# Kernel tuning notes

Measured on AMD Instinct MI355X. Metric: run time of the kernel, lower is better.

## Reference

```python
import jax, jax.numpy as jnp
import numpy as np

N, M, D = 32768, 4096, 256   # tokens, codebook_size, dim_feature
COMMITMENT_WEIGHT = 0.25


def setup_inputs() -> dict:
    key = jax.random.key(0)
    kx, ke = jax.random.split(key)
    x = jax.random.normal(kx, (N, D), dtype=jnp.float32)
    # learnable codebook (kaiming-uniform in torch; normal is fine for a numeric baseline)
    embed = jax.random.normal(ke, (M, D), dtype=jnp.float32) * (D ** -0.5)
    return {"x": x, "embed": embed}


def reference(x, embed):
    # argmin over squared distances == argmin over sqrt distances (monotone),
    # matching l2_dist(...).argmin(dim=1) in the original KeOps path.
    x2 = jnp.sum(x * x, axis=-1, keepdims=True)          # [N,1]
    e2 = jnp.sum(embed * embed, axis=-1)                 # [M]
    d2 = x2 - 2.0 * (x @ embed.T) + e2[None, :]          # [N,M]
    idx = jnp.argmin(d2, axis=1)                         # [N] code assignment

    q = embed[idx]                                       # codebook gather [N,D]

    # straight-through estimator: forward value is q, gradient flows to x
    quantized = x + jax.lax.stop_gradient(q - x)

    # commitment loss beta*||sg(x_q) - x||^2 + codebook loss ||x_q - sg(x)||^2
    commit_loss = COMMITMENT_WEIGHT * jnp.mean((jax.lax.stop_gradient(q) - x) ** 2)
    codebook_loss = jnp.mean((q - jax.lax.stop_gradient(x)) ** 2)
    loss = commit_loss + codebook_loss

    # cluster sizes via scatter-add (bincount) and perplexity
    counts = jnp.zeros((M,), jnp.float32).at[idx].add(1.0)
    probs = counts / counts.sum()
    perplexity = jnp.exp(-jnp.sum(probs * jnp.log(probs + 1e-10)))

    return quantized, idx, loss, perplexity
```

## Files before the change

### kernel.cpp

```cpp
#include <hip/hip_runtime.h>
#include <hip/hip_bf16.h>
#include <math.h>

#define NTOK 32768
#define MCB  4096
#define DDIM 256
#define NGATHER 8192

typedef __attribute__((ext_vector_type(8))) short bf16x8;
typedef __attribute__((ext_vector_type(4))) float f32x4;

__device__ __forceinline__ unsigned short f2bf_rne(float f) {
  unsigned int u = __float_as_uint(f);
  unsigned int r = u + 0x7FFFu + ((u >> 16) & 1u);
  return (unsigned short)(r >> 16);
}

__device__ __forceinline__ float bf2f(unsigned short h) {
  return __uint_as_float(((unsigned int)h) << 16);
}

__device__ __forceinline__ void cvt8(const float* f, bf16x8& hi, bf16x8& lo) {
  #pragma unroll
  for (int j = 0; j < 8; ++j) {
    unsigned short hs = f2bf_rne(f[j]);
    float lf = f[j] - bf2f(hs);
    hi[j] = (short)hs;
    lo[j] = (short)f2bf_rne(lf);
  }
}

__device__ __forceinline__ void load_lds16(const void* g, void* l) {
  __builtin_amdgcn_global_load_lds(
      (const __attribute__((address_space(1))) void*)g,
      (__attribute__((address_space(3))) void*)l, 16, 0, 0);
}

__global__ __launch_bounds__(256) void vq_prep_kernel(
    const float* __restrict__ embed, char* __restrict__ ehi,
    char* __restrict__ elo, float* __restrict__ e2) {
  const int id = blockIdx.x * 256 + threadIdx.x;
  const int row = id >> 5;
  const int c = id & 31;
  const float* ep = embed + (size_t)row * DDIM + c * 8;
  const float4 f0 = *(const float4*)(ep);
  const float4 f1 = *(const float4*)(ep + 4);
  float f[8] = {f0.x, f0.y, f0.z, f0.w, f1.x, f1.y, f1.z, f1.w};
  bf16x8 h, l;
  cvt8(f, h, l);
  const size_t off = (size_t)row * 512 + (size_t)(((c ^ (row & 7)) * 16));
  *(bf16x8*)(ehi + off) = h;
  *(bf16x8*)(elo + off) = l;
  float s = 0.0f;
  #pragma unroll
  for (int j = 0; j < 8; ++j) s += f[j] * f[j];
  #pragma unroll
  for (int m = 1; m < 32; m <<= 1) s += __shfl_xor(s, m, 64);
  if (c == 0) e2[row] = s;
}

__global__ __launch_bounds__(256, 2) void vq_main_kernel(
    const float* __restrict__ x, const char* __restrict__ ehi,
    const char* __restrict__ elo, const float* __restrict__ e2,
    float* __restrict__ ws_score, int* __restrict__ ws_idx) {
  __shared__ char lds[65536];
  const int tid = threadIdx.x;
  const int lane = tid & 63;
  const int wv = tid >> 6;
  const int split = blockIdx.x;
  const int row0 = blockIdx.y * 128 + wv * 32;
  const int colbase = split * 1024;
  const int l15 = lane & 15;
  const int l4 = lane >> 4;

  bf16x8 axh[2][8], axl[2][8];
  #pragma unroll
  for (int rf = 0; rf < 2; ++rf) {
    const float* xp = x + (size_t)(row0 + rf * 16 + l15) * DDIM + l4 * 8;
    #pragma unroll
    for (int ks = 0; ks < 8; ++ks) {
      float4 f0 = *(const float4*)(xp + ks * 32);
      float4 f1 = *(const float4*)(xp + ks * 32 + 4);
      float f[8] = {f0.x, f0.y, f0.z, f0.w, f1.x, f1.y, f1.z, f1.w};
      cvt8(f, axh[rf][ks], axl[rf][ks]);
    }
  }

  float minv[2][4];
  int mini[2][4];
  #pragma unroll
  for (int rf = 0; rf < 2; ++rf)
    #pragma unroll
    for (int r = 0; r < 4; ++r) { minv[rf][r] = 3.0e38f; mini[rf][r] = 0; }

  for (int ct = 0; ct < 16; ++ct) {
    __syncthreads();
    {
      const size_t tb = (size_t)(colbase + ct * 64) * 512 + (size_t)tid * 16;
      const char* ghi = ehi + tb;
      const char* glo = elo + tb;
      #pragma unroll
      for (int i = 0; i < 8; ++i) {
        load_lds16(ghi + i * 4096, lds + tid * 16 + i * 4096);
        load_lds16(glo + i * 4096, lds + 32768 + tid * 16 + i * 4096);
      }
    }
    __syncthreads();

    f32x4 acc[2][4];
    #pragma unroll
    for (int rf = 0; rf < 2; ++rf)
      #pragma unroll
      for (int cf = 0; cf < 4; ++cf) {
        f32x4 z = {0.0f, 0.0f, 0.0f, 0.0f};
        acc[rf][cf] = z;
      }

    #pragma unroll
    for (int ks = 0; ks < 8; ++ks) {
      bf16x8 bh[4], bl[4];
      #pragma unroll
      for (int cf = 0; cf < 4; ++cf) {
        const int brow = cf * 16 + l15;
        const int off = brow * 512 + (((ks * 4 + l4) ^ (brow & 7)) * 16);
        bh[cf] = *(const bf16x8*)(lds + off);
        bl[cf] = *(const bf16x8*)(lds + 32768 + off);
      }
      #pragma unroll
      for (int rf = 0; rf < 2; ++rf)
        #pragma unroll
        for (int cf = 0; cf < 4; ++cf) {
          f32x4 a = acc[rf][cf];
          a = __builtin_amdgcn_mfma_f32_16x16x32_bf16(axh[rf][ks], bh[cf], a, 0, 0, 0);
          a = __builtin_amdgcn_mfma_f32_16x16x32_bf16(axh[rf][ks], bl[cf], a, 0, 0, 0);
          a = __builtin_amdgcn_mfma_f32_16x16x32_bf16(axl[rf][ks], bh[cf], a, 0, 0, 0);
          acc[rf][cf] = a;
        }
    }

    #pragma unroll
    for (int cf = 0; cf < 4; ++cf) {
      const int col = colbase + ct * 64 + cf * 16 + l15;
      const float ee = e2[col];
      #pragma unroll
      for (int rf = 0; rf < 2; ++rf)
        #pragma unroll
        for (int r = 0; r < 4; ++r) {
          const float s = ee - 2.0f * acc[rf][cf][r];
          if (s < minv[rf][r]) { minv[rf][r] = s; mini[rf][r] = col; }
        }
    }
  }

  #pragma unroll
  for (int rf = 0; rf < 2; ++rf)
    #pragma unroll
    for (int r = 0; r < 4; ++r) {
      float s = minv[rf][r];
      int c = mini[rf][r];
      #pragma unroll
      for (int m = 1; m < 16; m <<= 1) {
        const float os = __shfl_xor(s, m, 64);
        const int oc = __shfl_xor(c, m, 64);
        if (os < s || (os == s && oc < c)) { s = os; c = oc; }
      }
      if (l15 == 0) {
        const int row = row0 + rf * 16 + l4 * 4 + r;
        ws_score[row * 4 + split] = s;
        ws_idx[row * 4 + split] = c;
      }
    }
}

__global__ void vq_merge_kernel(const float* __restrict__ ws_score,
                                const int* __restrict__ ws_idx,
                                int* __restrict__ minidx,
                                float* __restrict__ counts,
                                float* __restrict__ out_idx) {
  const int row = blockIdx.x * 256 + threadIdx.x;
  float bs = ws_score[row * 4];
  int bc = ws_idx[row * 4];
  #pragma unroll
  for (int s2 = 1; s2 < 4; ++s2) {
    const float s = ws_score[row * 4 + s2];
    const int c = ws_idx[row * 4 + s2];
    if (s < bs || (s == bs && c < bc)) { bs = s; bc = c; }
  }
  minidx[row] = bc;
  out_idx[row] = (float)bc;
  atomicAdd(&counts[bc], 1.0f);
}

__global__ __launch_bounds__(256) void vq_gather_kernel(
    const float* __restrict__ x, const float* __restrict__ embed,
    const int* __restrict__ minidx, float* __restrict__ outq,
    double* __restrict__ partials) {
  __shared__ double sh[4];
  const int lane = threadIdx.x & 63;
  const int wv = threadIdx.x >> 6;
  const int row = blockIdx.x * 4 + wv;
  const int idx = minidx[row];
  const float4 q4 = *(const float4*)(embed + (size_t)idx * DDIM + lane * 4);
  const float4 x4 = *(const float4*)(x + (size_t)row * DDIM + lane * 4);
  const float dx = q4.x - x4.x, dy = q4.y - x4.y, dz = q4.z - x4.z, dw = q4.w - x4.w;
  float4 o;
  o.x = x4.x + dx; o.y = x4.y + dy; o.z = x4.z + dz; o.w = x4.w + dw;
  *(float4*)(outq + (size_t)row * DDIM + lane * 4) = o;
  double ss = (double)(dx * dx) + (double)(dy * dy) + (double)(dz * dz) + (double)(dw * dw);
  #pragma unroll
  for (int m = 1; m < 64; m <<= 1) ss += __shfl_xor(ss, m, 64);
  if (lane == 0) sh[wv] = ss;
  __syncthreads();
  if (threadIdx.x == 0) partials[blockIdx.x] = sh[0] + sh[1] + sh[2] + sh[3];
}

__global__ void vq_fin_kernel(const float* __restrict__ counts,
                              const double* __restrict__ partials,
                              float* __restrict__ out) {
  __shared__ double sh[256];
  __shared__ double sl[256];
  double h = 0.0;
  for (int i = threadIdx.x; i < MCB; i += 256) {
    const float p = counts[i] * (1.0f / 32768.0f);
    h += (double)(p * logf(p + 1e-10f));
  }
  double ls = 0.0;
  for (int i = threadIdx.x; i < NGATHER; i += 256) ls += partials[i];
  sh[threadIdx.x] = h;
  sl[threadIdx.x] = ls;
  __syncthreads();
  for (int s = 128; s > 0; s >>= 1) {
    if (threadIdx.x < s) {
      sh[threadIdx.x] += sh[threadIdx.x + s];
      sl[threadIdx.x] += sl[threadIdx.x + s];
    }
    __syncthreads();
  }
  if (threadIdx.x == 0) {
    const size_t base = (size_t)NTOK * DDIM + NTOK;
    out[base] = (float)(1.25 * sl[0] / (double)((size_t)NTOK * DDIM));
    out[base + 1] = (float)exp(-sh[0]);
  }
}

extern "C" void kernel_launch(void* const* d_in, const int* in_sizes, int n_in,
                              void* d_out, int out_size, void* d_ws, size_t ws_size,
                              hipStream_t stream) {
  const float* x = (const float*)d_in[0];
  const float* embed = (const float*)d_in[1];
  float* out = (float*)d_out;
  char* ws = (char*)d_ws;

  float* ws_score = (float*)(ws);
  int* ws_idx = (int*)(ws + 0x80000);
  int* minidx = (int*)(ws + 0x100000);
  float* counts = (float*)(ws + 0x120000);
  double* partials = (double*)(ws + 0x128000);
  float* e2 = (float*)(ws + 0x138000);
  char* ehi = ws + 0x140000;
  char* elo = ws + 0x340000;

  hipMemsetAsync(ws + 0x120000, 0, 16384, stream);
  hipLaunchKernelGGL(vq_prep_kernel, dim3(512), dim3(256), 0, stream,
                     embed, ehi, elo, e2);
  hipLaunchKernelGGL(vq_main_kernel, dim3(4, 256), dim3(256), 0, stream,
                     x, ehi, elo, e2, ws_score, ws_idx);
  hipLaunchKernelGGL(vq_merge_kernel, dim3(128), dim3(256), 0, stream,
                     ws_score, ws_idx, minidx, counts, out + (size_t)NTOK * DDIM);
  hipLaunchKernelGGL(vq_gather_kernel, dim3(NGATHER), dim3(256), 0, stream,
                     x, embed, minidx, out, partials);
  hipLaunchKernelGGL(vq_fin_kernel, dim3(1), dim3(256), 0, stream,
                     counts, partials, out);
}
```

Before: 277.8 us.

## Pipeline codebook tiles through a four-slot LDS ring with async staging

Replaces the synchronous 64-column tile loop with 16-column tiles streamed through a four-slot LDS ring buffer. Loads are issued three tiles ahead, with explicit vmcnt waits and one barrier per tile, so global-to-LDS traffic overlaps the MFMA work. Codebook norms are cached in LDS, and the high and correction products go into separate accumulators to shorten MFMA dependency chains. The MFMA section also runs at raised wave priority. The risk is more barriers per unit of work, less MFMA work per tile to hide latency, and fragile hand-tuned waitcnt counts.

```diff
diff --git a/kernel.cpp b/kernel.cpp
--- a/kernel.cpp
+++ b/kernel.cpp
@@ -64,6 +64,7 @@
     const char* __restrict__ elo, const float* __restrict__ e2,
     float* __restrict__ ws_score, int* __restrict__ ws_idx) {
   __shared__ char lds[65536];
+  __shared__ float e2s[1024];
   const int tid = threadIdx.x;
   const int lane = tid & 63;
   const int wv = tid >> 6;
@@ -86,6 +87,8 @@
     }
   }
 
+  *(float4*)&e2s[tid * 4] = *(const float4*)&e2[colbase + tid * 4];
+
   float minv[2][4];
   int mini[2][4];
   #pragma unroll
@@ -93,63 +96,75 @@
     #pragma unroll
     for (int r = 0; r < 4; ++r) { minv[rf][r] = 3.0e38f; mini[rf][r] = 0; }
 
-  for (int ct = 0; ct < 16; ++ct) {
-    __syncthreads();
-    {
-      const size_t tb = (size_t)(colbase + ct * 64) * 512 + (size_t)tid * 16;
-      const char* ghi = ehi + tb;
-      const char* glo = elo + tb;
+  const int r3 = l15 & 3;
+  const int b = (l15 >> 2) & 1;
+  const int off_e = l15 * 512 + (l4 ^ r3) * 16 + b * 64;
+  const int off_o = off_e ^ 64;
+
+  const char* gh = ehi + (size_t)colbase * 512 + tid * 16;
+  const char* gl = elo + (size_t)colbase * 512 + tid * 16;
+  char* dst0 = &lds[tid * 16];
+
+  auto stage = [&](int ct, int bi) {
+    const char* sh_ = gh + ct * 8192;
+    const char* sl_ = gl + ct * 8192;
+    char* d = dst0 + bi * 16384;
+    load_lds16(sh_, d);
+    load_lds16(sh_ + 4096, d + 4096);
+    load_lds16(sl_, d + 8192);
+    load_lds16(sl_ + 4096, d + 12288);
+  };
+
+  auto body = [&](int t) {
+    const char* bp = lds + ((t & 3) << 14);
+    const float ee = e2s[t * 16 + l15];
+    f32x4 ah[2], ac[2];
+    #pragma unroll
+    for (int rf = 0; rf < 2; ++rf) {
+      f32x4 z = {0.0f, 0.0f, 0.0f, 0.0f};
+      ah[rf] = z; ac[rf] = z;
+    }
+    __builtin_amdgcn_s_setprio(1);
+    #pragma unroll
+    for (int ks = 0; ks < 8; ++ks) {
+      const int o = ((ks & 1) ? off_o : off_e) + (ks >> 1) * 128;
+      bf16x8 bh = *(const bf16x8*)(bp + o);
+      bf16x8 bl = *(const bf16x8*)(bp + o + 8192);
       #pragma unroll
-      for (int i = 0; i < 8; ++i) {
-        load_lds16(ghi + i * 4096, lds + tid * 16 + i * 4096);
-        load_lds16(glo + i * 4096, lds + 32768 + tid * 16 + i * 4096);
-      }
-    }
-    __syncthreads();
-
-    f32x4 acc[2][4];
+      for (int rf = 0; rf < 2; ++rf) {
+        ah[rf] = __builtin_amdgcn_mfma_f32_16x16x32_bf16(axh[rf][ks], bh, ah[rf], 0, 0, 0);
+        ac[rf] = __builtin_amdgcn_mfma_f32_16x16x32_bf16(axh[rf][ks], bl, ac[rf], 0, 0, 0);
+        ac[rf] = __builtin_amdgcn_mfma_f32_16x16x32_bf16(axl[rf][ks], bh, ac[rf], 0, 0, 0);
+      }
+    }
+    __builtin_amdgcn_s_setprio(0);
+    const int col = colbase + t * 16 + l15;
     #pragma unroll
     for (int rf = 0; rf < 2; ++rf)
       #pragma unroll
-      for (int cf = 0; cf < 4; ++cf) {
-        f32x4 z = {0.0f, 0.0f, 0.0f, 0.0f};
-        acc[rf][cf] = z;
-      }
-
-    #pragma unroll
-    for (int ks = 0; ks < 8; ++ks) {
-      bf16x8 bh[4], bl[4];
-      #pragma unroll
-      for (int cf = 0; cf < 4; ++cf) {
-        const int brow = cf * 16 + l15;
-        const int off = brow * 512 + (((ks * 4 + l4) ^ (brow & 7)) * 16);
-        bh[cf] = *(const bf16x8*)(lds + off);
-        bl[cf] = *(const bf16x8*)(lds + 32768 + off);
-      }
-      #pragma unroll
-      for (int rf = 0; rf < 2; ++rf)
-        #pragma unroll
-        for (int cf = 0; cf < 4; ++cf) {
-          f32x4 a = acc[rf][cf];
-          a = __builtin_amdgcn_mfma_f32_16x16x32_bf16(axh[rf][ks], bh[cf], a, 0, 0, 0);
-          a = __builtin_amdgcn_mfma_f32_16x16x32_bf16(axh[rf][ks], bl[cf], a, 0, 0, 0);
-          a = __builtin_amdgcn_mfma_f32_16x16x32_bf16(axl[rf][ks], bh[cf], a, 0, 0, 0);
-          acc[rf][cf] = a;
-        }
-    }
-
-    #pragma unroll
-    for (int cf = 0; cf < 4; ++cf) {
-      const int col = colbase + ct * 64 + cf * 16 + l15;
-      const float ee = e2[col];
-      #pragma unroll
-      for (int rf = 0; rf < 2; ++rf)
-        #pragma unroll
-        for (int r = 0; r < 4; ++r) {
-          const float s = ee - 2.0f * acc[rf][cf][r];
-          if (s < minv[rf][r]) { minv[rf][r] = s; mini[rf][r] = col; }
-        }
-    }
+      for (int r = 0; r < 4; ++r) {
+        const float d = ah[rf][r] + ac[rf][r];
+        const float s = fmaf(-2.0f, d, ee);
+        if (s < minv[rf][r]) { minv[rf][r] = s; mini[rf][r] = col; }
+      }
+  };
+
+  stage(0, 0);
+  stage(1, 1);
+  stage(2, 2);
+  __syncthreads();
+
+  for (int t = 0; t < 64; ++t) {
+    if (t >= 3) {
+      if (t <= 61)      asm volatile("s_waitcnt vmcnt(8)" ::: "memory");
+      else if (t == 62) asm volatile("s_waitcnt vmcnt(4)" ::: "memory");
+      else              asm volatile("s_waitcnt vmcnt(0)" ::: "memory");
+      __builtin_amdgcn_sched_barrier(0);
+    }
+    __builtin_amdgcn_s_barrier();
+    __builtin_amdgcn_sched_barrier(0);
+    if (t <= 60) stage(t + 3, (t + 3) & 3);
+    body(t);
   }
 
   #pragma unroll
```

Result: slower. 308.0 us (+10.9%).
